# Kernel optimization log

Hardware: AMD Instinct MI355X
Metric: run time of the kernel (lower is better)

The kernel has to match this reference:

```python
import jax, jax.numpy as jnp
import numpy as np

DECAY = 0.99
EPS = 1e-05


def setup_inputs() -> dict:
    key = jax.random.key(0)
    k1, k2, k3, k4 = jax.random.split(key, 4)
    B, T, D, K = 16, 4096, 128, 1024
    return {
        "z": jax.random.normal(k1, (B, T, D), dtype=jnp.float32),
        "embedding": jax.random.normal(k2, (K, D), dtype=jnp.float32),
        "cluster_size": jax.random.uniform(k3, (K,), dtype=jnp.float32),
        "ema_w": jax.random.normal(k4, (K, D), dtype=jnp.float32),
    }


def reference(z, embedding, cluster_size, ema_w):
    B, T, D = z.shape
    K = embedding.shape[0]
    z_flat = z.reshape(B * T, D)

    # Squared-distance matrix [N, K]: ||z||^2 - 2 z E^T + ||E||^2
    dist = (
        jnp.sum(z_flat * z_flat, axis=1, keepdims=True)
        - 2.0 * (z_flat @ embedding.T)
        + jnp.sum(embedding * embedding, axis=1)
    )
    indices = jnp.argmin(dist, axis=1)  # [N]
    z_q = embedding[indices].reshape(B, T, D)

    # EMA codebook update (training branch); segment_sum == one_hot.T @ z, one_hot.sum(0)
    batch_cluster = jax.ops.segment_sum(
        jnp.ones((B * T,), dtype=z.dtype), indices, num_segments=K
    )
    new_cluster_size = cluster_size * DECAY + (1.0 - DECAY) * batch_cluster
    batch_ema = jax.ops.segment_sum(z_flat, indices, num_segments=K)
    new_ema_w = ema_w * DECAY + (1.0 - DECAY) * batch_ema

    n = jnp.sum(new_cluster_size)
    smoothed = (new_cluster_size + EPS) / (n + K * EPS) * n
    new_embedding = new_ema_w / smoothed[:, None]

    # Commitment loss on OLD codebook vectors (matches torch order of ops)
    loss_vq = jnp.mean(jnp.square(jax.lax.stop_gradient(z_q) - z))
    # Straight-through estimator
    z_q_st = z + jax.lax.stop_gradient(z_q - z)

    return (
        z_q_st,
        indices.reshape(B, T),
        loss_vq,
        new_embedding,
        new_cluster_size,
        new_ema_w,
    )
```

## Files before the change

kernel.cpp:

```cpp
#include <hip/hip_runtime.h>

#define K_CODES 1024
#define D_DIM 128
#define N_ROWS 65536
#define DECAY_F 0.99f
#define OMD_F 0.01f
#define EPS_F 1e-5f

#define EPAD 136
#define CHUNK_CODES 128
#define N_CHUNKS (K_CODES / CHUNK_CODES)
#define CHUNK_USHORT (2 * CHUNK_CODES * EPAD)

#define SEG_TILE 64

#define WS_ENORM  0
#define WS_SMOOTH 1024
#define WS_BE     2048
#define WS_CNT    133120
#define WS_LOSS   134144
#define WS_CUR    134160
#define WS_FIDX   135184
#define WS_I12    200720
#define WS_BUCKET 331792
#define WS_SCODE  397328
#define WS_EIMG   462864

typedef __bf16 bf8_t __attribute__((ext_vector_type(8)));
typedef float  f4_t  __attribute__((ext_vector_type(4)));

__device__ inline unsigned short f2bf_bits(float f) {
    __bf16 h = (__bf16)f;
    return __builtin_bit_cast(unsigned short, h);
}
__device__ inline float bf_bits2f(unsigned short u) {
    __bf16 h = __builtin_bit_cast(__bf16, u);
    return (float)h;
}

__global__ void vq_enorm(const float* __restrict__ emb, float* __restrict__ enorm) {
    int k = blockIdx.x * blockDim.x + threadIdx.x;
    if (k >= K_CODES) return;
    const float4* e4 = (const float4*)(emb + (size_t)k * D_DIM);
    float s = 0.f;
#pragma unroll
    for (int i = 0; i < D_DIM / 4; ++i) {
        float4 v = e4[i];
        s += v.x * v.x + v.y * v.y + v.z * v.z + v.w * v.w;
    }
    enorm[k] = s;
}

__global__ void vq_esplit(const float* __restrict__ emb, unsigned short* __restrict__ eimg) {
    int t = blockIdx.x * blockDim.x + threadIdx.x;
    int code = t >> 5;
    int q = t & 31;
    float4 v = ((const float4*)(emb + (size_t)code * D_DIM))[q];
    int chunk = code >> 7, c = code & 127;
    size_t hbase = (size_t)chunk * CHUNK_USHORT + (size_t)c * EPAD + q * 4;
    size_t lbase = hbase + (size_t)CHUNK_CODES * EPAD;
    float vv[4] = {v.x, v.y, v.z, v.w};
    ushort4 hi, lo;
    unsigned short* hp = (unsigned short*)&hi;
    unsigned short* lp = (unsigned short*)&lo;
#pragma unroll
    for (int i = 0; i < 4; ++i) {
        unsigned short hb = f2bf_bits(vv[i]);
        hp[i] = hb;
        lp[i] = f2bf_bits(vv[i] - bf_bits2f(hb));
    }
    *(ushort4*)(eimg + hbase) = hi;
    *(ushort4*)(eimg + lbase) = lo;
}

__device__ inline void top2_update(float s, int code, float& s1, int& i1, float& s2, int& i2) {
    bool b1 = s < s1;
    bool b2 = s < s2;
    s2 = b1 ? s1 : (b2 ? s : s2);
    i2 = b1 ? i1 : (b2 ? code : i2);
    s1 = b1 ? s : s1;
    i1 = b1 ? code : i1;
}

__device__ inline void top2_merge(float& s1, int& i1, float& s2, int& i2,
                                  float t1, int j1, float t2, int j2) {
    bool bf = (t1 < s1) || (t1 == s1 && j1 < i1);
    float ns1 = bf ? t1 : s1;  int ni1 = bf ? j1 : i1;
    float ca  = bf ? s1 : t1;  int ia  = bf ? i1 : j1;
    float cb  = bf ? t2 : s2;  int ib  = bf ? j2 : i2;
    bool bs = (ca < cb) || (ca == cb && ia < ib);
    s1 = ns1; i1 = ni1;
    s2 = bs ? ca : cb; i2 = bs ? ia : ib;
}

__global__ __launch_bounds__(256, 2) void vq_score(
    const float* __restrict__ z, const unsigned short* __restrict__ eimg,
    const float* __restrict__ enorm, unsigned int* __restrict__ i12)
{
    __shared__ __align__(16) unsigned short lds[CHUNK_USHORT];
    __shared__ float lds_en[CHUNK_CODES];

    const int tid  = threadIdx.x;
    const int wv   = tid >> 6;
    const int lane = tid & 63;
    const int l16  = lane & 15;
    const int quad = lane >> 4;

    bf8_t zh[2][4], zl[2][4];
#pragma unroll
    for (int nt = 0; nt < 2; ++nt) {
        int row = blockIdx.x * 128 + wv * 32 + nt * 16 + l16;
        const float* zr = z + (size_t)row * D_DIM;
#pragma unroll
        for (int ks = 0; ks < 4; ++ks) {
            const float4* p = (const float4*)(zr + ks * 32 + quad * 8);
            float4 a = p[0], b = p[1];
            float v[8] = {a.x, a.y, a.z, a.w, b.x, b.y, b.z, b.w};
#pragma unroll
            for (int i = 0; i < 8; ++i) {
                __bf16 hh = (__bf16)v[i];
                zh[nt][ks][i] = hh;
                zl[nt][ks][i] = (__bf16)(v[i] - (float)hh);
            }
        }
    }

    float s1[2] = {3.4e38f, 3.4e38f}, s2[2] = {3.4e38f, 3.4e38f};
    int   i1[2] = {0, 0},             i2[2] = {0, 0};

    for (int chunk = 0; chunk < N_CHUNKS; ++chunk) {
        __syncthreads();
        {
            const uint4* src = (const uint4*)(eimg + (size_t)chunk * CHUNK_USHORT);
            uint4* dst = (uint4*)lds;
#pragma unroll
            for (int i = 0; i < 17; ++i) dst[tid + 256 * i] = src[tid + 256 * i];
            if (tid < CHUNK_CODES) lds_en[tid] = enorm[chunk * CHUNK_CODES + tid];
        }
        __syncthreads();

#pragma unroll
        for (int cg = 0; cg < 2; ++cg) {
            f4_t acc[4][2];
#pragma unroll
            for (int ct = 0; ct < 4; ++ct)
#pragma unroll
                for (int nt = 0; nt < 2; ++nt) acc[ct][nt] = (f4_t)(0.f);

#pragma unroll
            for (int ks = 0; ks < 4; ++ks) {
                bf8_t ah[4], al[4];
#pragma unroll
                for (int ct = 0; ct < 4; ++ct) {
                    int cl = cg * 64 + ct * 16 + l16;
                    int base = cl * EPAD + ks * 32 + quad * 8;
                    ah[ct] = *(const bf8_t*)&lds[base];
                    al[ct] = *(const bf8_t*)&lds[CHUNK_CODES * EPAD + base];
                }
#pragma unroll
                for (int ct = 0; ct < 4; ++ct)
#pragma unroll
                    for (int nt = 0; nt < 2; ++nt) {
                        acc[ct][nt] = __builtin_amdgcn_mfma_f32_16x16x32_bf16(
                            ah[ct], zh[nt][ks], acc[ct][nt], 0, 0, 0);
                        acc[ct][nt] = __builtin_amdgcn_mfma_f32_16x16x32_bf16(
                            al[ct], zh[nt][ks], acc[ct][nt], 0, 0, 0);
                        acc[ct][nt] = __builtin_amdgcn_mfma_f32_16x16x32_bf16(
                            ah[ct], zl[nt][ks], acc[ct][nt], 0, 0, 0);
                    }
            }

#pragma unroll
            for (int ct = 0; ct < 4; ++ct)
#pragma unroll
                for (int nt = 0; nt < 2; ++nt)
#pragma unroll
                    for (int r = 0; r < 4; ++r) {
                        int cl = cg * 64 + ct * 16 + quad * 4 + r;
                        float s = lds_en[cl] - 2.0f * acc[ct][nt][r];
                        int code = chunk * CHUNK_CODES + cl;
                        top2_update(s, code, s1[nt], i1[nt], s2[nt], i2[nt]);
                    }
        }
    }

#pragma unroll
    for (int off = 16; off <= 32; off <<= 1) {
#pragma unroll
        for (int nt = 0; nt < 2; ++nt) {
            float t1 = __shfl_xor(s1[nt], off, 64);
            int   j1 = __shfl_xor(i1[nt], off, 64);
            float t2 = __shfl_xor(s2[nt], off, 64);
            int   j2 = __shfl_xor(i2[nt], off, 64);
            top2_merge(s1[nt], i1[nt], s2[nt], i2[nt], t1, j1, t2, j2);
        }
    }

    if (lane < 16) {
#pragma unroll
        for (int nt = 0; nt < 2; ++nt) {
            int row = blockIdx.x * 128 + wv * 32 + nt * 16 + l16;
            i12[2 * row]     = (unsigned int)i1[nt];
            i12[2 * row + 1] = (unsigned int)i2[nt];
        }
    }
}

__global__ __launch_bounds__(256) void vq_decide(
    const float* __restrict__ z, const float* __restrict__ emb,
    const float* __restrict__ enorm, const unsigned int* __restrict__ i12,
    float* __restrict__ out_zq, float* __restrict__ out_idx,
    int* __restrict__ cnt, unsigned int* __restrict__ fidx,
    float* __restrict__ loss_acc)
{
    const int tid  = threadIdx.x;
    const int half = tid & 1;
    const int row  = blockIdx.x * 128 + (tid >> 1);

    float4 zr[16];
    const float4* zp = (const float4*)(z + (size_t)row * D_DIM + half * 64);
#pragma unroll
    for (int i = 0; i < 16; ++i) zr[i] = zp[i];

    int j1 = (int)i12[2 * row];
    int j2 = (int)i12[2 * row + 1];

    const float4* e1 = (const float4*)(emb + (size_t)j1 * D_DIM + half * 64);
    const float4* e2 = (const float4*)(emb + (size_t)j2 * D_DIM + half * 64);
    float p1 = 0.f, p2 = 0.f;
#pragma unroll
    for (int i = 0; i < 16; ++i) {
        float4 a = e1[i], b = e2[i], zv = zr[i];
        p1 += zv.x * a.x + zv.y * a.y + zv.z * a.z + zv.w * a.w;
        p2 += zv.x * b.x + zv.y * b.y + zv.z * b.z + zv.w * b.w;
    }
    float d1 = p1 + __shfl_xor(p1, 1, 64);
    float d2 = p2 + __shfl_xor(p2, 1, 64);
    float sc1 = enorm[j1] - 2.0f * d1;
    float sc2 = enorm[j2] - 2.0f * d2;
    int best = (sc2 < sc1 || (sc2 == sc1 && j2 < j1)) ? j2 : j1;

    if (half == 0) {
        out_idx[row] = (float)best;
        fidx[row] = (unsigned int)best;
        atomicAdd(cnt + best, 1);
    }

    const float4* eq = (const float4*)(emb + (size_t)best * D_DIM + half * 64);
    float4* oz = (float4*)(out_zq + (size_t)row * D_DIM + half * 64);

    float ls = 0.f;
#pragma unroll
    for (int i = 0; i < 16; ++i) {
        float4 q = eq[i], zv = zr[i];
        float4 df = {q.x - zv.x, q.y - zv.y, q.z - zv.z, q.w - zv.w};
        ls += df.x * df.x + df.y * df.y + df.z * df.z + df.w * df.w;
        float4 o = {zv.x + df.x, zv.y + df.y, zv.z + df.z, zv.w + df.w};
        oz[i] = o;
    }

#pragma unroll
    for (int off = 32; off > 0; off >>= 1) ls += __shfl_down(ls, off, 64);
    if ((tid & 63) == 0) atomicAdd(loss_acc, ls);
}

__global__ void vq_scan(const int* __restrict__ cnt, int* __restrict__ cursor)
{
    __shared__ int tmp[K_CODES];
    int k = threadIdx.x;
    int c = cnt[k];
    tmp[k] = c;
    __syncthreads();
    for (int off = 1; off < K_CODES; off <<= 1) {
        int t = (k >= off) ? tmp[k - off] : 0;
        __syncthreads();
        tmp[k] += t;
        __syncthreads();
    }
    cursor[k] = tmp[k] - c;
}

__global__ void vq_scatter(const unsigned int* __restrict__ fidx,
                           int* __restrict__ cursor, unsigned int* __restrict__ bucket,
                           int* __restrict__ scode)
{
    int row = blockIdx.x * blockDim.x + threadIdx.x;
    int k = (int)fidx[row];
    int slot = atomicAdd(cursor + k, 1);
    bucket[slot] = (unsigned int)row;
    scode[slot]  = k;
}

__global__ __launch_bounds__(128) void vq_segsum(
    const float* __restrict__ z, const unsigned int* __restrict__ bucket,
    const int* __restrict__ scode, float* __restrict__ be)
{
    __shared__ int sb[SEG_TILE];
    __shared__ int sc[SEG_TILE];
    const int tid = threadIdx.x;
    const int t0  = blockIdx.x * SEG_TILE;

    if (tid < SEG_TILE) sb[tid] = (int)bucket[t0 + tid];
    else if (tid < 2 * SEG_TILE) sc[tid - SEG_TILE] = scode[t0 + tid - SEG_TILE];
    __syncthreads();

    const int d = tid;
    float acc = 0.f;
    int cur = sc[0];

    for (int i = 0; i < SEG_TILE; i += 8) {
        float v[8];
#pragma unroll
        for (int j = 0; j < 8; ++j)
            v[j] = z[(size_t)sb[i + j] * D_DIM + d];
#pragma unroll
        for (int j = 0; j < 8; ++j) {
            int c = sc[i + j];
            if (c != cur) {
                atomicAdd(be + (size_t)cur * D_DIM + d, acc);
                acc = 0.f;
                cur = c;
            }
            acc += v[j];
        }
    }
    atomicAdd(be + (size_t)cur * D_DIM + d, acc);
}

__global__ void vq_finalize1(const float* __restrict__ cs, const int* __restrict__ cnt,
                             const float* __restrict__ loss_acc,
                             float* __restrict__ out_ncs, float* __restrict__ out_loss,
                             float* __restrict__ smoothed)
{
    __shared__ float red[K_CODES];
    int k = threadIdx.x;
    float ncs = cs[k] * DECAY_F + OMD_F * (float)cnt[k];
    out_ncs[k] = ncs;
    red[k] = ncs;
    __syncthreads();
    for (int s = 512; s > 0; s >>= 1) {
        if (k < s) red[k] += red[k + s];
        __syncthreads();
    }
    float n = red[0];
    smoothed[k] = (ncs + EPS_F) / (n + (float)K_CODES * EPS_F) * n;
    if (k == 0) out_loss[0] = loss_acc[0] / (float)((size_t)N_ROWS * D_DIM);
}

__global__ void vq_finalize2(const float* __restrict__ ema_w, const float* __restrict__ be,
                             const float* __restrict__ smoothed,
                             float* __restrict__ out_emb, float* __restrict__ out_ema)
{
    int i = blockIdx.x * blockDim.x + threadIdx.x;
    float e = ema_w[i] * DECAY_F + OMD_F * be[i];
    out_ema[i] = e;
    out_emb[i] = e / smoothed[i >> 7];
}

extern "C" void kernel_launch(void* const* d_in, const int* in_sizes, int n_in,
                              void* d_out, int out_size, void* d_ws, size_t ws_size,
                              hipStream_t stream) {
    const float* z   = (const float*)d_in[0];
    const float* emb = (const float*)d_in[1];
    const float* cs  = (const float*)d_in[2];
    const float* ema = (const float*)d_in[3];

    float* out    = (float*)d_out;
    float* o_zq   = out;
    float* o_idx  = o_zq + (size_t)N_ROWS * D_DIM;
    float* o_loss = o_idx + N_ROWS;
    float* o_emb  = o_loss + 1;
    float* o_ncs  = o_emb + K_CODES * D_DIM;
    float* o_ema  = o_ncs + K_CODES;

    float* ws = (float*)d_ws;
    float*          enorm    = ws + WS_ENORM;
    float*          smoothed = ws + WS_SMOOTH;
    float*          be       = ws + WS_BE;
    int*            cnt      = (int*)(ws + WS_CNT);
    float*          lacc     = ws + WS_LOSS;
    int*            cursor   = (int*)(ws + WS_CUR);
    unsigned int*   fidx     = (unsigned int*)(ws + WS_FIDX);
    unsigned int*   i12      = (unsigned int*)(ws + WS_I12);
    unsigned int*   bucket   = (unsigned int*)(ws + WS_BUCKET);
    int*            scode    = (int*)(ws + WS_SCODE);
    unsigned short* eimg     = (unsigned short*)(ws + WS_EIMG);

    hipMemsetAsync(ws + WS_CNT, 0, (K_CODES + 1) * sizeof(float), stream);
    hipMemsetAsync(ws + WS_BE, 0, (size_t)K_CODES * D_DIM * sizeof(float), stream);
    vq_enorm<<<4, 256, 0, stream>>>(emb, enorm);
    vq_esplit<<<128, 256, 0, stream>>>(emb, eimg);
    vq_score<<<N_ROWS / 128, 256, 0, stream>>>(z, eimg, enorm, i12);
    vq_decide<<<N_ROWS / 128, 256, 0, stream>>>(z, emb, enorm, i12,
                                                o_zq, o_idx, cnt, fidx, lacc);
    vq_scan<<<1, K_CODES, 0, stream>>>(cnt, cursor);
    vq_scatter<<<N_ROWS / 256, 256, 0, stream>>>(fidx, cursor, bucket, scode);
    vq_segsum<<<N_ROWS / SEG_TILE, 128, 0, stream>>>(z, bucket, scode, be);
    vq_finalize1<<<1, K_CODES, 0, stream>>>(cs, cnt, lacc, o_ncs, o_loss, smoothed);
    vq_finalize2<<<K_CODES * D_DIM / 256, 256, 0, stream>>>(ema, be, smoothed, o_emb, o_ema);
}
```

Before: 248.8 us.

## Fuse score and decide kernels with double-buffered async codebook loads

Merges the top-2 scoring kernel and the exact fp32 re-check/output kernel into one, which removes the i12 round trip and one launch. The norm and bf16-split prep kernels become one, and the two memsets become one. In the score kernel each block now handles 256 rows with NT=4 row tiles per wave over 256 blocks, and the codebook chunks are double-buffered in LDS through global_load_lds so loads overlap the MFMA work. The trade-off is more registers and twice the LDS per block, with the launch-bounds occupancy hint dropped. The grid also shrinks to 256 blocks, which may underfill the GPU.

```diff
diff --git a/kernel.cpp b/kernel.cpp
--- a/kernel.cpp
+++ b/kernel.cpp
@@ -9,22 +9,22 @@
 
 #define EPAD 136
 #define CHUNK_CODES 128
-#define N_CHUNKS (K_CODES / CHUNK_CODES)
+#define N_CHUNKS 8
 #define CHUNK_USHORT (2 * CHUNK_CODES * EPAD)
-
+#define NT 4
 #define SEG_TILE 64
 
-#define WS_ENORM  0
-#define WS_SMOOTH 1024
-#define WS_BE     2048
-#define WS_CNT    133120
-#define WS_LOSS   134144
-#define WS_CUR    134160
-#define WS_FIDX   135184
-#define WS_I12    200720
-#define WS_BUCKET 331792
-#define WS_SCODE  397328
-#define WS_EIMG   462864
+#define WS_CNT     0
+#define WS_LOSS    1024
+#define WS_BE      1028
+#define WS_ZERO_END (1028 + 131072)
+#define WS_ENORM   132100
+#define WS_SMOOTH  133124
+#define WS_CUR     134148
+#define WS_FIDX    135172
+#define WS_BUCKET  200708
+#define WS_SCODE   266244
+#define WS_EIMG    331780
 
 typedef __bf16 bf8_t __attribute__((ext_vector_type(8)));
 typedef float  f4_t  __attribute__((ext_vector_type(4)));
@@ -38,20 +38,14 @@
     return (float)h;
 }
 
-__global__ void vq_enorm(const float* __restrict__ emb, float* __restrict__ enorm) {
-    int k = blockIdx.x * blockDim.x + threadIdx.x;
-    if (k >= K_CODES) return;
-    const float4* e4 = (const float4*)(emb + (size_t)k * D_DIM);
-    float s = 0.f;
-#pragma unroll
-    for (int i = 0; i < D_DIM / 4; ++i) {
-        float4 v = e4[i];
-        s += v.x * v.x + v.y * v.y + v.z * v.z + v.w * v.w;
-    }
-    enorm[k] = s;
-}
-
-__global__ void vq_esplit(const float* __restrict__ emb, unsigned short* __restrict__ eimg) {
+__device__ inline void gld16(const void* g, void* l) {
+    __builtin_amdgcn_global_load_lds(
+        (const __attribute__((address_space(1))) void*)g,
+        (__attribute__((address_space(3))) void*)l, 16, 0, 0);
+}
+
+__global__ void vq_prep(const float* __restrict__ emb, float* __restrict__ enorm,
+                        unsigned short* __restrict__ eimg) {
     int t = blockIdx.x * blockDim.x + threadIdx.x;
     int code = t >> 5;
     int q = t & 31;
@@ -71,6 +65,11 @@
     }
     *(ushort4*)(eimg + hbase) = hi;
     *(ushort4*)(eimg + lbase) = lo;
+
+    float s = v.x * v.x + v.y * v.y + v.z * v.z + v.w * v.w;
+#pragma unroll
+    for (int o = 1; o < 32; o <<= 1) s += __shfl_xor(s, o, 64);
+    if (q == 0) enorm[code] = s;
 }
 
 __device__ inline void top2_update(float s, int code, float& s1, int& i1, float& s2, int& i2) {
@@ -93,23 +92,38 @@
     s2 = bs ? ca : cb; i2 = bs ? ia : ib;
 }
 
-__global__ __launch_bounds__(256, 2) void vq_score(
+__global__ __launch_bounds__(256) void vq_score(
     const float* __restrict__ z, const unsigned short* __restrict__ eimg,
-    const float* __restrict__ enorm, unsigned int* __restrict__ i12)
-{
-    __shared__ __align__(16) unsigned short lds[CHUNK_USHORT];
-    __shared__ float lds_en[CHUNK_CODES];
+    const float* __restrict__ enorm_g, const float* __restrict__ emb,
+    float* __restrict__ out_zq, float* __restrict__ out_idx,
+    int* __restrict__ cnt, unsigned int* __restrict__ fidx,
+    float* __restrict__ loss_acc)
+{
+    __shared__ __align__(16) unsigned short lds[2][CHUNK_USHORT];
+    __shared__ __align__(16) float lds_en[K_CODES];
 
     const int tid  = threadIdx.x;
     const int wv   = tid >> 6;
     const int lane = tid & 63;
     const int l16  = lane & 15;
     const int quad = lane >> 4;
-
-    bf8_t zh[2][4], zl[2][4];
-#pragma unroll
-    for (int nt = 0; nt < 2; ++nt) {
-        int row = blockIdx.x * 128 + wv * 32 + nt * 16 + l16;
+    const int rowbase = blockIdx.x * 256 + wv * 64;
+
+    ((float4*)lds_en)[tid] = ((const float4*)enorm_g)[tid];
+
+    {
+        const char* gs = (const char*)eimg;
+        char* ls = (char*)&lds[0][0];
+        int wb = wv * 17408;
+#pragma unroll
+        for (int i = 0; i < 17; ++i)
+            gld16(gs + wb + i * 1024 + lane * 16, ls + wb + i * 1024);
+    }
+
+    bf8_t zh[NT][4], zl[NT][4];
+#pragma unroll
+    for (int nt = 0; nt < NT; ++nt) {
+        int row = rowbase + nt * 16 + l16;
         const float* zr = z + (size_t)row * D_DIM;
 #pragma unroll
         for (int ks = 0; ks < 4; ++ks) {
@@ -125,42 +139,47 @@
         }
     }
 
-    float s1[2] = {3.4e38f, 3.4e38f}, s2[2] = {3.4e38f, 3.4e38f};
-    int   i1[2] = {0, 0},             i2[2] = {0, 0};
-
-    for (int chunk = 0; chunk < N_CHUNKS; ++chunk) {
-        __syncthreads();
-        {
-            const uint4* src = (const uint4*)(eimg + (size_t)chunk * CHUNK_USHORT);
-            uint4* dst = (uint4*)lds;
-#pragma unroll
-            for (int i = 0; i < 17; ++i) dst[tid + 256 * i] = src[tid + 256 * i];
-            if (tid < CHUNK_CODES) lds_en[tid] = enorm[chunk * CHUNK_CODES + tid];
-        }
-        __syncthreads();
-
-#pragma unroll
-        for (int cg = 0; cg < 2; ++cg) {
-            f4_t acc[4][2];
-#pragma unroll
-            for (int ct = 0; ct < 4; ++ct)
-#pragma unroll
-                for (int nt = 0; nt < 2; ++nt) acc[ct][nt] = (f4_t)(0.f);
+    float s1[NT], s2[NT];
+    int   i1[NT], i2[NT];
+#pragma unroll
+    for (int nt = 0; nt < NT; ++nt) { s1[nt] = 3.4e38f; s2[nt] = 3.4e38f; i1[nt] = 0; i2[nt] = 0; }
+
+    __syncthreads();
+
+    for (int c = 0; c < N_CHUNKS; ++c) {
+        const int cur = c & 1;
+        if (c + 1 < N_CHUNKS) {
+            const char* gs = (const char*)(eimg + (size_t)(c + 1) * CHUNK_USHORT);
+            char* ls = (char*)&lds[1 - cur][0];
+            int wb = wv * 17408;
+#pragma unroll
+            for (int i = 0; i < 17; ++i)
+                gld16(gs + wb + i * 1024 + lane * 16, ls + wb + i * 1024);
+        }
+        const unsigned short* buf = &lds[cur][0];
+
+#pragma unroll
+        for (int cg = 0; cg < 4; ++cg) {
+            f4_t acc[2][NT];
+#pragma unroll
+            for (int ct = 0; ct < 2; ++ct)
+#pragma unroll
+                for (int nt = 0; nt < NT; ++nt) acc[ct][nt] = (f4_t)(0.f);
 
 #pragma unroll
             for (int ks = 0; ks < 4; ++ks) {
-                bf8_t ah[4], al[4];
-#pragma unroll
-                for (int ct = 0; ct < 4; ++ct) {
-                    int cl = cg * 64 + ct * 16 + l16;
+                bf8_t ah[2], al[2];
+#pragma unroll
+                for (int ct = 0; ct < 2; ++ct) {
+                    int cl = cg * 32 + ct * 16 + l16;
                     int base = cl * EPAD + ks * 32 + quad * 8;
-                    ah[ct] = *(const bf8_t*)&lds[base];
-                    al[ct] = *(const bf8_t*)&lds[CHUNK_CODES * EPAD + base];
+                    ah[ct] = *(const bf8_t*)&buf[base];
+                    al[ct] = *(const bf8_t*)&buf[CHUNK_CODES * EPAD + base];
                 }
 #pragma unroll
-                for (int ct = 0; ct < 4; ++ct)
-#pragma unroll
-                    for (int nt = 0; nt < 2; ++nt) {
+                for (int ct = 0; ct < 2; ++ct)
+#pragma unroll
+                    for (int nt = 0; nt < NT; ++nt) {
                         acc[ct][nt] = __builtin_amdgcn_mfma_f32_16x16x32_bf16(
                             ah[ct], zh[nt][ks], acc[ct][nt], 0, 0, 0);
                         acc[ct][nt] = __builtin_amdgcn_mfma_f32_16x16x32_bf16(
@@ -171,23 +190,26 @@
             }
 
 #pragma unroll
-            for (int ct = 0; ct < 4; ++ct)
-#pragma unroll
-                for (int nt = 0; nt < 2; ++nt)
+            for (int ct = 0; ct < 2; ++ct) {
+                int cb = c * 128 + cg * 32 + ct * 16 + quad * 4;
+                float4 en4 = *(const float4*)&lds_en[cb];
+                float env[4] = {en4.x, en4.y, en4.z, en4.w};
+#pragma unroll
+                for (int nt = 0; nt < NT; ++nt)
 #pragma unroll
                     for (int r = 0; r < 4; ++r) {
-                        int cl = cg * 64 + ct * 16 + quad * 4 + r;
-                        float s = lds_en[cl] - 2.0f * acc[ct][nt][r];
-                        int code = chunk * CHUNK_CODES + cl;
-                        top2_update(s, code, s1[nt], i1[nt], s2[nt], i2[nt]);
+                        float s = env[r] - 2.0f * acc[ct][nt][r];
+                        top2_update(s, cb + r, s1[nt], i1[nt], s2[nt], i2[nt]);
                     }
-        }
+            }
+        }
+        __syncthreads();
     }
 
 #pragma unroll
     for (int off = 16; off <= 32; off <<= 1) {
 #pragma unroll
-        for (int nt = 0; nt < 2; ++nt) {
+        for (int nt = 0; nt < NT; ++nt) {
             float t1 = __shfl_xor(s1[nt], off, 64);
             int   j1 = __shfl_xor(i1[nt], off, 64);
             float t2 = __shfl_xor(s2[nt], off, 64);
@@ -196,72 +218,58 @@
         }
     }
 
-    if (lane < 16) {
-#pragma unroll
-        for (int nt = 0; nt < 2; ++nt) {
-            int row = blockIdx.x * 128 + wv * 32 + nt * 16 + l16;
-            i12[2 * row]     = (unsigned int)i1[nt];
-            i12[2 * row + 1] = (unsigned int)i2[nt];
-        }
-    }
-}
-
-__global__ __launch_bounds__(256) void vq_decide(
-    const float* __restrict__ z, const float* __restrict__ emb,
-    const float* __restrict__ enorm, const unsigned int* __restrict__ i12,
-    float* __restrict__ out_zq, float* __restrict__ out_idx,
-    int* __restrict__ cnt, unsigned int* __restrict__ fidx,
-    float* __restrict__ loss_acc)
-{
-    const int tid  = threadIdx.x;
-    const int half = tid & 1;
-    const int row  = blockIdx.x * 128 + (tid >> 1);
-
-    float4 zr[16];
-    const float4* zp = (const float4*)(z + (size_t)row * D_DIM + half * 64);
-#pragma unroll
-    for (int i = 0; i < 16; ++i) zr[i] = zp[i];
-
-    int j1 = (int)i12[2 * row];
-    int j2 = (int)i12[2 * row + 1];
-
-    const float4* e1 = (const float4*)(emb + (size_t)j1 * D_DIM + half * 64);
-    const float4* e2 = (const float4*)(emb + (size_t)j2 * D_DIM + half * 64);
-    float p1 = 0.f, p2 = 0.f;
-#pragma unroll
-    for (int i = 0; i < 16; ++i) {
-        float4 a = e1[i], b = e2[i], zv = zr[i];
-        p1 += zv.x * a.x + zv.y * a.y + zv.z * a.z + zv.w * a.w;
-        p2 += zv.x * b.x + zv.y * b.y + zv.z * b.z + zv.w * b.w;
-    }
-    float d1 = p1 + __shfl_xor(p1, 1, 64);
-    float d2 = p2 + __shfl_xor(p2, 1, 64);
-    float sc1 = enorm[j1] - 2.0f * d1;
-    float sc2 = enorm[j2] - 2.0f * d2;
-    int best = (sc2 < sc1 || (sc2 == sc1 && j2 < j1)) ? j2 : j1;
-
-    if (half == 0) {
-        out_idx[row] = (float)best;
-        fidx[row] = (unsigned int)best;
-        atomicAdd(cnt + best, 1);
-    }
-
-    const float4* eq = (const float4*)(emb + (size_t)best * D_DIM + half * 64);
-    float4* oz = (float4*)(out_zq + (size_t)row * D_DIM + half * 64);
-
     float ls = 0.f;
 #pragma unroll
-    for (int i = 0; i < 16; ++i) {
-        float4 q = eq[i], zv = zr[i];
-        float4 df = {q.x - zv.x, q.y - zv.y, q.z - zv.z, q.w - zv.w};
-        ls += df.x * df.x + df.y * df.y + df.z * df.z + df.w * df.w;
-        float4 o = {zv.x + df.x, zv.y + df.y, zv.z + df.z, zv.w + df.w};
-        oz[i] = o;
+    for (int nt = 0; nt < NT; ++nt) {
+        int row = rowbase + nt * 16 + l16;
+        int j1 = i1[nt], j2 = i2[nt];
+
+        const float4* zp  = (const float4*)(z   + (size_t)row * D_DIM);
+        const float4* e1p = (const float4*)(emb + (size_t)j1  * D_DIM);
+        const float4* e2p = (const float4*)(emb + (size_t)j2  * D_DIM);
+
+        float4 zv[8], a1[8], a2[8];
+#pragma unroll
+        for (int ks = 0; ks < 4; ++ks) {
+            int o = ks * 8 + quad * 2;
+            zv[ks * 2]     = zp[o];   zv[ks * 2 + 1] = zp[o + 1];
+            a1[ks * 2]     = e1p[o];  a1[ks * 2 + 1] = e1p[o + 1];
+            a2[ks * 2]     = e2p[o];  a2[ks * 2 + 1] = e2p[o + 1];
+        }
+        float p1 = 0.f, p2 = 0.f;
+#pragma unroll
+        for (int i = 0; i < 8; ++i) {
+            p1 += zv[i].x * a1[i].x + zv[i].y * a1[i].y + zv[i].z * a1[i].z + zv[i].w * a1[i].w;
+            p2 += zv[i].x * a2[i].x + zv[i].y * a2[i].y + zv[i].z * a2[i].z + zv[i].w * a2[i].w;
+        }
+        p1 += __shfl_xor(p1, 16, 64); p1 += __shfl_xor(p1, 32, 64);
+        p2 += __shfl_xor(p2, 16, 64); p2 += __shfl_xor(p2, 32, 64);
+        float sc1 = lds_en[j1] - 2.0f * p1;
+        float sc2 = lds_en[j2] - 2.0f * p2;
+        bool use2 = (sc2 < sc1) || (sc2 == sc1 && j2 < j1);
+        int best = use2 ? j2 : j1;
+
+        if (quad == 0) {
+            out_idx[row] = (float)best;
+            fidx[row] = (unsigned int)best;
+            atomicAdd(cnt + best, 1);
+        }
+
+        float4* oz = (float4*)(out_zq + (size_t)row * D_DIM);
+#pragma unroll
+        for (int i = 0; i < 8; ++i) {
+            float4 q = use2 ? a2[i] : a1[i];
+            float4 zvv = zv[i];
+            float4 df = {q.x - zvv.x, q.y - zvv.y, q.z - zvv.z, q.w - zvv.w};
+            ls += df.x * df.x + df.y * df.y + df.z * df.z + df.w * df.w;
+            float4 o = {zvv.x + df.x, zvv.y + df.y, zvv.z + df.z, zvv.w + df.w};
+            oz[(i >> 1) * 8 + quad * 2 + (i & 1)] = o;
+        }
     }
 
 #pragma unroll
     for (int off = 32; off > 0; off >>= 1) ls += __shfl_down(ls, off, 64);
-    if ((tid & 63) == 0) atomicAdd(loss_acc, ls);
+    if (lane == 0) atomicAdd(loss_acc, ls);
 }
 
 __global__ void vq_scan(const int* __restrict__ cnt, int* __restrict__ cursor)
@@ -374,25 +382,21 @@
     float* o_ema  = o_ncs + K_CODES;
 
     float* ws = (float*)d_ws;
+    int*            cnt      = (int*)(ws + WS_CNT);
+    float*          lacc     = ws + WS_LOSS;
+    float*          be       = ws + WS_BE;
     float*          enorm    = ws + WS_ENORM;
     float*          smoothed = ws + WS_SMOOTH;
-    float*          be       = ws + WS_BE;
-    int*            cnt      = (int*)(ws + WS_CNT);
-    float*          lacc     = ws + WS_LOSS;
     int*            cursor   = (int*)(ws + WS_CUR);
     unsigned int*   fidx     = (unsigned int*)(ws + WS_FIDX);
-    unsigned int*   i12      = (unsigned int*)(ws + WS_I12);
     unsigned int*   bucket   = (unsigned int*)(ws + WS_BUCKET);
     int*            scode    = (int*)(ws + WS_SCODE);
     unsigned short* eimg     = (unsigned short*)(ws + WS_EIMG);
 
-    hipMemsetAsync(ws + WS_CNT, 0, (K_CODES + 1) * sizeof(float), stream);
-    hipMemsetAsync(ws + WS_BE, 0, (size_t)K_CODES * D_DIM * sizeof(float), stream);
-    vq_enorm<<<4, 256, 0, stream>>>(emb, enorm);
-    vq_esplit<<<128, 256, 0, stream>>>(emb, eimg);
-    vq_score<<<N_ROWS / 128, 256, 0, stream>>>(z, eimg, enorm, i12);
-    vq_decide<<<N_ROWS / 128, 256, 0, stream>>>(z, emb, enorm, i12,
-                                                o_zq, o_idx, cnt, fidx, lacc);
+    hipMemsetAsync(ws, 0, (size_t)WS_ZERO_END * sizeof(float), stream);
+    vq_prep<<<128, 256, 0, stream>>>(emb, enorm, eimg);
+    vq_score<<<256, 256, 0, stream>>>(z, eimg, enorm, emb,
+                                      o_zq, o_idx, cnt, fidx, lacc);
     vq_scan<<<1, K_CODES, 0, stream>>>(cnt, cursor);
     vq_scatter<<<N_ROWS / 256, 256, 0, stream>>>(fidx, cursor, bucket, scode);
     vq_segsum<<<N_ROWS / SEG_TILE, 128, 0, stream>>>(z, bucket, scode, be);
```

Result: faster. 222.9 us (-10.4%).
